# Kernel optimization log

Hardware: AMD Instinct MI355X
Metric: run time of the kernel (lower is better)

## Reference

```python
import jax, jax.numpy as jnp
import numpy as np

MIN_DISTANCE = 1.0
CONSTRAINT_WEIGHT = 0.02


def setup_inputs() -> dict:
    key = jax.random.key(0)
    pos = jax.random.normal(key, (16384, 3), dtype=jnp.float32) * 5.0
    return {"pos": pos}


def reference(pos):
    # pos: [N, 3]
    n = pos.shape[0]
    # Pairwise Euclidean distances via the gram trick (avoids [N,N,3] diff tensor)
    sq = jnp.sum(pos * pos, axis=-1)                      # [N]
    d2 = sq[:, None] + sq[None, :] - 2.0 * (pos @ pos.T)  # [N, N]
    d2 = jnp.maximum(d2, 0.0)
    eye = jnp.eye(n, dtype=bool)
    # keep sqrt away from 0 on the diagonal (masked to inf anyway)
    dist = jnp.sqrt(jnp.where(eye, 1.0, d2))
    dist = jnp.where(eye, jnp.inf, dist)                  # masked_fill(eye, inf)
    violations = jnp.maximum(MIN_DISTANCE - dist, 0.0)    # clamp(min=0)
    constraint_loss = jnp.mean(violations) * CONSTRAINT_WEIGHT
    return pos, constraint_loss
```

## Files before the change

kernel.cpp:

```cpp
#include <hip/hip_runtime.h>


constexpr int   N     = 16384;
constexpr int   BLOCK = 256;
constexpr int   GSZ   = 512;
constexpr int   IPT   = GSZ / BLOCK;
constexpr int   NG    = N / GSZ;
constexpr int   F     = 8;
constexpr int   NB    = NG * F;
constexpr int   QB    = 4;
constexpr int   NBINS = 256;
constexpr float BINW_INV = 4.0f;
constexpr int   MARGIN = 6;
constexpr int   CH    = 288;
constexpr int   NHB   = N / BLOCK;

__device__ __forceinline__ int zcell(float z) {
    int c = (int)floorf(z * BINW_INV) + NBINS / 2;
    return min(max(c, 0), NBINS - 1);
}

__global__ void __launch_bounds__(BLOCK)
prep_kernel(const float* __restrict__ pos, float* __restrict__ out,
            unsigned int* __restrict__ histPart, unsigned int* __restrict__ crk,
            float* __restrict__ acc, unsigned int* __restrict__ cnt) {
    __shared__ unsigned int lh[NBINS];
    const int b = blockIdx.x, t = threadIdx.x;
    const int gt = b * BLOCK + t;
    lh[t] = 0u;
    if (gt == 0) { *acc = 0.0f; *cnt = 0u; }
    __syncthreads();
    if (gt < (N * 3) / 4) {
        reinterpret_cast<float4*>(out)[gt] = reinterpret_cast<const float4*>(pos)[gt];
    }
    const float z = pos[3 * gt + 2];
    const int cell = zcell(z);
    const unsigned int rank = atomicAdd(&lh[cell], 1u);
    crk[gt] = (unsigned int)cell | (rank << 16);
    __syncthreads();
    histPart[b * NBINS + t] = lh[t];
}

__global__ void __launch_bounds__(BLOCK)
scatter_kernel(const float* __restrict__ pos, const unsigned int* __restrict__ histPart,
               const unsigned int* __restrict__ crk, float4* __restrict__ jt4s,
               int* __restrict__ jendArr) {
    __shared__ int sm[NBINS];
    __shared__ int beforeB[NBINS];
    const int b = blockIdx.x, t = threadIdx.x;
    int v = 0, bef = 0;
    #pragma unroll 8
    for (int p = 0; p < NHB; ++p) {
        const int hv = (int)histPart[p * NBINS + t];
        if (p == b) bef = v;
        v += hv;
    }
    sm[t] = v; beforeB[t] = bef;
    __syncthreads();
    for (int off = 1; off < NBINS; off <<= 1) {
        const int a = (t >= off) ? sm[t - off] : 0;
        __syncthreads();
        sm[t] += a;
        __syncthreads();
    }
    const int gt = b * BLOCK + t;
    const unsigned int cr = crk[gt];
    const int cell = (int)(cr & 0xffffu);
    const int rank = (int)(cr >> 16);
    const int ex   = (cell > 0) ? sm[cell - 1] : 0;
    const int dst  = ex + beforeB[cell] + rank;
    const float x = pos[3 * gt], y = pos[3 * gt + 1], z = pos[3 * gt + 2];
    jt4s[dst] = make_float4(x, y, z, fmaf(x, x, fmaf(y, y, z * z)));
    if (b == 0 && t < NG) {
        const int p = (t + 1) * GSZ - 1;
        int lo = 0, hi = NBINS - 1;
        while (lo < hi) {
            const int mid = (lo + hi) >> 1;
            if (sm[mid] >= p + 1) hi = mid; else lo = mid + 1;
        }
        const int jidx = lo + MARGIN;
        jendArr[t] = (jidx >= NBINS) ? N : sm[jidx - 1];
    }
}

template <bool MASKED>
__device__ __forceinline__ float cols(const float4* __restrict__ jsm,
                                      int clen, int jbase, int i0,
                                      const float (&xi2)[IPT], const float (&yi2)[IPT],
                                      const float (&zi2)[IPT], const float (&sqi)[IPT]) {
    float s = 0.0f;
    for (int c = 0; c < clen; c += QB) {
        #pragma unroll
        for (int u = 0; u < QB; ++u) {
            const float4 pj = jsm[c + u];
            const int jq = jbase + c + u;
            #pragma unroll
            for (int k = 0; k < IPT; ++k) {
                float d = fmaf(xi2[k], pj.x, pj.w);
                d = fmaf(yi2[k], pj.y, d);
                d = fmaf(zi2[k], pj.z, d);
                const float d2 = fmaxf(d + sqi[k], 0.0f);
                float w = 1.0f - __builtin_amdgcn_sqrtf(d2);
                w = fmaxf(w, 0.0f);
                if (MASKED) w = (jq > i0 + k * BLOCK) ? w : 0.0f;
                s += w;
            }
        }
    }
    return s;
}

__global__ void __launch_bounds__(BLOCK)
pair_kernel(const float4* __restrict__ jt4s, const int* __restrict__ jendArr,
            float* __restrict__ out, float* __restrict__ acc,
            unsigned int* __restrict__ cnt) {
    __shared__ float4 jsm[CH + QB];
    __shared__ float wsum[BLOCK / 64];
    const int b = blockIdx.x;
    const int t = threadIdx.x;
    const int g = b >> 3, f = b & (F - 1);
    const int gstart = g * GSZ;
    const int i0 = gstart + t;

    const float4 w0 = jt4s[i0];
    const float4 w1 = jt4s[i0 + BLOCK];

    const int jend = jendArr[g];
    const int jbeg = gstart + 1;
    const int jlen = jend - jbeg;
    const int seg  = (((jlen + F - 1) / F) + QB - 1) & ~(QB - 1);
    const int j0   = jbeg + f * seg;
    const int len  = min(seg, jend - j0);

    float xi2[IPT], yi2[IPT], zi2[IPT], sqi[IPT];
    xi2[0] = -2.0f * w0.x; yi2[0] = -2.0f * w0.y; zi2[0] = -2.0f * w0.z; sqi[0] = w0.w;
    xi2[1] = -2.0f * w1.x; yi2[1] = -2.0f * w1.y; zi2[1] = -2.0f * w1.z; sqi[1] = w1.w;

    float s = 0.0f;
    for (int cs = 0; cs < len; cs += CH) {
        const int clen = min(CH, len - cs);
        if (t < clen)         jsm[t]         = jt4s[j0 + cs + t];
        if (t + BLOCK < clen) jsm[t + BLOCK] = jt4s[j0 + cs + t + BLOCK];
        if (t < QB) jsm[clen + t] = make_float4(0.0f, 0.0f, 1.0e6f, 4.0e12f);
        __syncthreads();
        if (j0 + cs < gstart + GSZ)
            s += cols<true >(jsm, clen, j0 + cs, i0, xi2, yi2, zi2, sqi);
        else
            s += cols<false>(jsm, clen, j0 + cs, i0, xi2, yi2, zi2, sqi);
        __syncthreads();
    }

    for (int off = 32; off > 0; off >>= 1) s += __shfl_down(s, off);
    if ((t & 63) == 0) wsum[t >> 6] = s;
    __syncthreads();
    if (t == 0) {
        float bs = 0.0f;
        #pragma unroll
        for (int w = 0; w < BLOCK / 64; ++w) bs += wsum[w];
        atomicAdd(acc, bs);
        __threadfence();
        const unsigned int done = atomicAdd(cnt, 1u);
        if (done == (unsigned int)(NB - 1)) {
            __threadfence();
            const float total = atomicAdd(acc, 0.0f);
            const double mean = 2.0 * (double)total / ((double)N * (double)N);
            out[(size_t)N * 3] = (float)(mean * 0.02);
        }
    }
}

extern "C" void kernel_launch(void* const* d_in, const int* in_sizes, int n_in,
                              void* d_out, int out_size, void* d_ws, size_t ws_size,
                              hipStream_t stream) {
    const float* pos = (const float*)d_in[0];
    float* out = (float*)d_out;
    float*        acc      = (float*)d_ws;
    unsigned int* cnt      = (unsigned int*)d_ws + 1;
    int*          jendArr  = (int*)((char*)d_ws + 256);
    unsigned int* histPart = (unsigned int*)((char*)d_ws + 4096);
    unsigned int* crk      = (unsigned int*)((char*)d_ws + 69632);
    float4*       jt4s     = (float4*)((char*)d_ws + 135168);

    prep_kernel   <<<NHB, BLOCK, 0, stream>>>(pos, out, histPart, crk, acc, cnt);
    scatter_kernel<<<NHB, BLOCK, 0, stream>>>(pos, histPart, crk, jt4s, jendArr);
    pair_kernel   <<<NB,  BLOCK, 0, stream>>>(jt4s, jendArr, out, acc, cnt);
}
```

Baseline: 82.00 us.

## Fuse scatter into pair kernel with a grid-wide atomic barrier

```diff
diff --git a/kernel.cpp b/kernel.cpp
--- a/kernel.cpp
+++ b/kernel.cpp
@@ -23,12 +23,13 @@
 __global__ void __launch_bounds__(BLOCK)
 prep_kernel(const float* __restrict__ pos, float* __restrict__ out,
             unsigned int* __restrict__ histPart, unsigned int* __restrict__ crk,
-            float* __restrict__ acc, unsigned int* __restrict__ cnt) {
+            float* __restrict__ acc, unsigned int* __restrict__ cnt,
+            unsigned int* __restrict__ bar) {
     __shared__ unsigned int lh[NBINS];
     const int b = blockIdx.x, t = threadIdx.x;
     const int gt = b * BLOCK + t;
     lh[t] = 0u;
-    if (gt == 0) { *acc = 0.0f; *cnt = 0u; }
+    if (gt == 0) { *acc = 0.0f; *cnt = 0u; *bar = 0u; }
     __syncthreads();
     if (gt < (N * 3) / 4) {
         reinterpret_cast<float4*>(out)[gt] = reinterpret_cast<const float4*>(pos)[gt];
@@ -39,48 +40,6 @@
     crk[gt] = (unsigned int)cell | (rank << 16);
     __syncthreads();
     histPart[b * NBINS + t] = lh[t];
-}
-
-__global__ void __launch_bounds__(BLOCK)
-scatter_kernel(const float* __restrict__ pos, const unsigned int* __restrict__ histPart,
-               const unsigned int* __restrict__ crk, float4* __restrict__ jt4s,
-               int* __restrict__ jendArr) {
-    __shared__ int sm[NBINS];
-    __shared__ int beforeB[NBINS];
-    const int b = blockIdx.x, t = threadIdx.x;
-    int v = 0, bef = 0;
-    #pragma unroll 8
-    for (int p = 0; p < NHB; ++p) {
-        const int hv = (int)histPart[p * NBINS + t];
-        if (p == b) bef = v;
-        v += hv;
-    }
-    sm[t] = v; beforeB[t] = bef;
-    __syncthreads();
-    for (int off = 1; off < NBINS; off <<= 1) {
-        const int a = (t >= off) ? sm[t - off] : 0;
-        __syncthreads();
-        sm[t] += a;
-        __syncthreads();
-    }
-    const int gt = b * BLOCK + t;
-    const unsigned int cr = crk[gt];
-    const int cell = (int)(cr & 0xffffu);
-    const int rank = (int)(cr >> 16);
-    const int ex   = (cell > 0) ? sm[cell - 1] : 0;
-    const int dst  = ex + beforeB[cell] + rank;
-    const float x = pos[3 * gt], y = pos[3 * gt + 1], z = pos[3 * gt + 2];
-    jt4s[dst] = make_float4(x, y, z, fmaf(x, x, fmaf(y, y, z * z)));
-    if (b == 0 && t < NG) {
-        const int p = (t + 1) * GSZ - 1;
-        int lo = 0, hi = NBINS - 1;
-        while (lo < hi) {
-            const int mid = (lo + hi) >> 1;
-            if (sm[mid] >= p + 1) hi = mid; else lo = mid + 1;
-        }
-        const int jidx = lo + MARGIN;
-        jendArr[t] = (jidx >= NBINS) ? N : sm[jidx - 1];
-    }
 }
 
 template <bool MASKED>
@@ -111,21 +70,72 @@
 }
 
 __global__ void __launch_bounds__(BLOCK)
-pair_kernel(const float4* __restrict__ jt4s, const int* __restrict__ jendArr,
-            float* __restrict__ out, float* __restrict__ acc,
-            unsigned int* __restrict__ cnt) {
+fused_kernel(const float* __restrict__ pos, const unsigned int* __restrict__ histPart,
+             const unsigned int* __restrict__ crk, float4* __restrict__ jt4s,
+             unsigned int* __restrict__ bar, float* __restrict__ out,
+             float* __restrict__ acc, unsigned int* __restrict__ cnt) {
+    __shared__ int sm[NBINS];
+    __shared__ int beforeB[NBINS];
     __shared__ float4 jsm[CH + QB];
     __shared__ float wsum[BLOCK / 64];
-    const int b = blockIdx.x;
-    const int t = threadIdx.x;
+    const int b = blockIdx.x, t = threadIdx.x;
+
+    const int pb = b >> 2;
+    int v = 0, bef = 0;
+    #pragma unroll 8
+    for (int p = 0; p < NHB; ++p) {
+        const int hv = (int)histPart[p * NBINS + t];
+        if (p == pb) bef = v;
+        v += hv;
+    }
+    sm[t] = v; beforeB[t] = bef;
+    __syncthreads();
+    for (int off = 1; off < NBINS; off <<= 1) {
+        const int a = (t >= off) ? sm[t - off] : 0;
+        __syncthreads();
+        sm[t] += a;
+        __syncthreads();
+    }
+
+    if (t < 64) {
+        const int gt = b * 64 + t;
+        const unsigned int cr = crk[gt];
+        const int cell = (int)(cr & 0xffffu);
+        const int rank = (int)(cr >> 16);
+        const int ex   = (cell > 0) ? sm[cell - 1] : 0;
+        const int dst  = ex + beforeB[cell] + rank;
+        const float x = pos[3 * gt], y = pos[3 * gt + 1], z = pos[3 * gt + 2];
+        jt4s[dst] = make_float4(x, y, z, fmaf(x, x, fmaf(y, y, z * z)));
+    }
+
     const int g = b >> 3, f = b & (F - 1);
+    int jend;
+    {
+        const int p = (g + 1) * GSZ - 1;
+        int lo = 0, hi = NBINS - 1;
+        while (lo < hi) {
+            const int mid = (lo + hi) >> 1;
+            if (sm[mid] >= p + 1) hi = mid; else lo = mid + 1;
+        }
+        const int jidx = lo + MARGIN;
+        jend = (jidx >= NBINS) ? N : sm[jidx - 1];
+    }
+
+    __syncthreads();
+    if (t == 0) {
+        __threadfence();
+        __hip_atomic_fetch_add(bar, 1u, __ATOMIC_ACQ_REL, __HIP_MEMORY_SCOPE_AGENT);
+        while (__hip_atomic_load(bar, __ATOMIC_ACQUIRE, __HIP_MEMORY_SCOPE_AGENT)
+               < (unsigned int)NB) { }
+        __threadfence();
+    }
+    __syncthreads();
+
     const int gstart = g * GSZ;
     const int i0 = gstart + t;
-
     const float4 w0 = jt4s[i0];
     const float4 w1 = jt4s[i0 + BLOCK];
 
-    const int jend = jendArr[g];
     const int jbeg = gstart + 1;
     const int jlen = jend - jbeg;
     const int seg  = (((jlen + F - 1) / F) + QB - 1) & ~(QB - 1);
@@ -176,12 +186,11 @@
     float* out = (float*)d_out;
     float*        acc      = (float*)d_ws;
     unsigned int* cnt      = (unsigned int*)d_ws + 1;
-    int*          jendArr  = (int*)((char*)d_ws + 256);
+    unsigned int* bar      = (unsigned int*)d_ws + 2;
     unsigned int* histPart = (unsigned int*)((char*)d_ws + 4096);
     unsigned int* crk      = (unsigned int*)((char*)d_ws + 69632);
     float4*       jt4s     = (float4*)((char*)d_ws + 135168);
 
-    prep_kernel   <<<NHB, BLOCK, 0, stream>>>(pos, out, histPart, crk, acc, cnt);
-    scatter_kernel<<<NHB, BLOCK, 0, stream>>>(pos, histPart, crk, jt4s, jendArr);
-    pair_kernel   <<<NB,  BLOCK, 0, stream>>>(jt4s, jendArr, out, acc, cnt);
+    prep_kernel <<<NHB, BLOCK, 0, stream>>>(pos, out, histPart, crk, acc, cnt, bar);
+    fused_kernel<<<NB,  BLOCK, 0, stream>>>(pos, histPart, crk, jt4s, bar, out, acc, cnt);
 }
```

After: 96.76 us. 18.0% more time.
